# Kernel tuning notes

Hardware: AMD Instinct MI355X
Metric: run time of the kernel (lower is better)

The kernel has to match this reference:

```python
import jax, jax.numpy as jnp
import numpy as np

K_TOP = 2        # experts_per_tok
E_MLP = 8        # num_mlp_experts


def setup_inputs() -> dict:
    key = jax.random.key(0)
    ks = jax.random.split(key, 6)
    B, T, C, H, E_ve, V = 2, 2048, 1024, 2048, 2, 32000
    return {
        "x": jax.random.normal(ks[0], (B, T, C), dtype=jnp.float32),
        "token_ids": jax.random.randint(ks[1], (B, T), 0, V, dtype=jnp.int32),
        "w_up": jax.random.normal(ks[2], (E_MLP, H, C), dtype=jnp.float32) * 0.02,
        "w_down": jax.random.normal(ks[3], (E_MLP, C, H), dtype=jnp.float32) * 0.02,
        "router_w": jax.random.normal(ks[4], (E_MLP + E_ve, C), dtype=jnp.float32) * 0.02,
        "router_bias": jnp.zeros((E_MLP + E_ve,), dtype=jnp.float32),
        "ve_tables": jax.random.normal(ks[5], (E_ve, V, C), dtype=jnp.float32) * 0.02,
    }


def reference(x, token_ids, w_up, w_down, router_w, router_bias, ve_tables):
    B, T, C = x.shape
    N = B * T
    E_total = router_w.shape[0]
    x_flat = x.reshape(N, C)

    # Sigmoid router with aux-loss-free bias (DeepSeekV3 style): select top-k on
    # biased scores, gate with unbiased sigmoid scores normalized over the top-k.
    scores = jax.nn.sigmoid(x_flat @ router_w.T)              # (N, E_total)
    _, top_idx = jax.lax.top_k(scores + router_bias, K_TOP)   # (N, k)
    top_w = jnp.take_along_axis(scores, top_idx, axis=1)      # (N, k)
    top_w = top_w / jnp.sum(top_w, axis=1, keepdims=True)

    rows = jnp.arange(N)[:, None]
    sparse_w = jnp.zeros((N, E_total), dtype=x.dtype).at[rows, top_idx].set(top_w)

    # Dense all-expert FFN (relu^2 activation), then mask by routing weights.
    hidden = jnp.einsum('nc,ehc->enh', x_flat, w_up)          # (E_mlp, N, H)
    hidden = jnp.square(jax.nn.relu(hidden))
    mlp_out = jnp.einsum('enh,ech->enc', hidden, w_down)      # (E_mlp, N, C)
    mlp_contrib = jnp.einsum('enc,ne->nc', mlp_out, sparse_w[:, :E_MLP])

    # VE experts: shared embedding lookups, (E_ve, N, C).
    ve_out = ve_tables[:, token_ids.reshape(N), :]
    ve_contrib = jnp.einsum('enc,ne->nc', ve_out, sparse_w[:, E_MLP:])

    return (mlp_contrib + ve_contrib).reshape(B, T, C)
```

## Files before the change

### kernel.cpp

```cpp
#include <hip/hip_runtime.h>
#include <hip/hip_bf16.h>
#include <stdint.h>

#define N_TOK 4096
#define C_DIM 1024
#define H_DIM 2048
#define V_DIM 32000
#define NE_MLP 8
#define NE_TOT 10

typedef __attribute__((ext_vector_type(8))) short bf16x8;
typedef __attribute__((ext_vector_type(4))) short bf16x4;
typedef __attribute__((ext_vector_type(4))) float f32x4;

#define BM 128
#define BN 128
#define BK 32

__device__ __forceinline__ void gload16(const void* g, void* l) {
    __builtin_amdgcn_global_load_lds(
        (const __attribute__((address_space(1))) void*)g,
        (__attribute__((address_space(3))) void*)l,
        16, 0, 0);
}

__device__ __forceinline__ unsigned short bf16bits(float v) {
    __hip_bfloat16 h = __float2bfloat16(v);
    return *reinterpret_cast<unsigned short*>(&h);
}

__global__ void __launch_bounds__(256) cvt_kernel(
    const float* __restrict__ src, __hip_bfloat16* __restrict__ dst)
{
    const int i = blockIdx.x * 256 + threadIdx.x;
    f32x4 v = reinterpret_cast<const f32x4*>(src)[i];
    bf16x4 b;
    b.x = (short)bf16bits(v.x); b.y = (short)bf16bits(v.y);
    b.z = (short)bf16bits(v.z); b.w = (short)bf16bits(v.w);
    reinterpret_cast<bf16x4*>(dst)[i] = b;
}

__global__ void __launch_bounds__(256) router_kernel(
    const float* __restrict__ x, const float* __restrict__ rw,
    const float* __restrict__ rb, int* __restrict__ tok_list,
    int* __restrict__ te, int* __restrict__ tp, float* __restrict__ tw,
    float* __restrict__ vw, int* __restrict__ cnt)
{
    const int lane = threadIdx.x & 63;
    const int n = blockIdx.x * 4 + (threadIdx.x >> 6);
    const f32x4* xr  = reinterpret_cast<const f32x4*>(x + (size_t)n * C_DIM);
    const f32x4* rw4 = reinterpret_cast<const f32x4*>(rw);

    float acc[NE_TOT];
    #pragma unroll
    for (int e = 0; e < NE_TOT; ++e) acc[e] = 0.f;

    #pragma unroll
    for (int kk = 0; kk < C_DIM / 256; ++kk) {
        f32x4 xv = xr[kk * 64 + lane];
        #pragma unroll
        for (int e = 0; e < NE_TOT; ++e) {
            f32x4 wv = rw4[e * (C_DIM / 4) + kk * 64 + lane];
            acc[e] += xv.x * wv.x + xv.y * wv.y + xv.z * wv.z + xv.w * wv.w;
        }
    }
    #pragma unroll
    for (int e = 0; e < NE_TOT; ++e) {
        for (int m = 32; m > 0; m >>= 1) acc[e] += __shfl_xor(acc[e], m, 64);
    }

    if (lane == 0) {
        float s[NE_TOT], sb[NE_TOT];
        #pragma unroll
        for (int e = 0; e < NE_TOT; ++e) {
            s[e]  = 1.f / (1.f + expf(-acc[e]));
            sb[e] = s[e] + rb[e];
        }
        int i0 = 0;
        #pragma unroll
        for (int e = 1; e < NE_TOT; ++e) if (sb[e] > sb[i0]) i0 = e;
        int i1 = (i0 == 0) ? 1 : 0;
        #pragma unroll
        for (int e = 0; e < NE_TOT; ++e)
            if (e != i0 && sb[e] > sb[i1]) i1 = e;

        float w0 = s[i0], w1 = s[i1];
        float inv = 1.f / (w0 + w1);
        w0 *= inv; w1 *= inv;

        float wv0 = 0.f, wv1 = 0.f;
        int   idx[2] = {i0, i1};
        float wt[2]  = {w0, w1};
        #pragma unroll
        for (int k = 0; k < 2; ++k) {
            if (idx[k] < NE_MLP) {
                int p = atomicAdd(&cnt[idx[k]], 1);
                tok_list[idx[k] * N_TOK + p] = n;
                te[n * 2 + k] = idx[k];
                tp[n * 2 + k] = p;
                tw[n * 2 + k] = wt[k];
            } else {
                te[n * 2 + k] = -1;
                tp[n * 2 + k] = 0;
                tw[n * 2 + k] = 0.f;
                if (idx[k] == NE_MLP) wv0 = wt[k]; else wv1 = wt[k];
            }
        }
        vw[n * 2 + 0] = wv0;
        vw[n * 2 + 1] = wv1;
    }
}

__global__ void scan_kernel(const int* __restrict__ cnt, int* __restrict__ offs)
{
    if (threadIdx.x == 0) {
        int o = 0;
        for (int e = 0; e < NE_MLP; ++e) { offs[e] = o; o += cnt[e]; }
    }
}

__global__ void __launch_bounds__(256) up_kernel(
    const __hip_bfloat16* __restrict__ xb, const __hip_bfloat16* __restrict__ wub,
    const int* __restrict__ tok_list, const int* __restrict__ cnt,
    const int* __restrict__ offs, __hip_bfloat16* __restrict__ hidden)
{
    const int e = blockIdx.z;
    const int count = cnt[e];
    const int m0 = blockIdx.y * BM;
    if (m0 >= count) return;
    const int n0 = blockIdx.x * BN;
    const int base = offs[e];

    __shared__ __hip_bfloat16 lA[BM * BK];
    __shared__ __hip_bfloat16 lB[BN * BK];

    const int tid  = threadIdx.x;
    const int lane = tid & 63;
    const int wv   = tid >> 6;
    const int wm = (wv >> 1) * 64;
    const int wn = (wv & 1) * 64;

    const __hip_bfloat16* ga[2];
    const __hip_bfloat16* gb[2];
    __hip_bfloat16* la[2];
    __hip_bfloat16* lb[2];
    const __hip_bfloat16* wB = wub + (size_t)e * H_DIM * C_DIM;
    #pragma unroll
    for (int t = 0; t < 2; ++t) {
        const int srow = (wv + 4 * t) * 16 + (lane >> 2);
        int r = m0 + srow;
        const int tok = tok_list[e * N_TOK + (r < count ? r : count - 1)];
        ga[t] = xb + (size_t)tok * C_DIM + (lane & 3) * 8;
        gb[t] = wB + (size_t)(n0 + srow) * C_DIM + (lane & 3) * 8;
        la[t] = lA + (wv + 4 * t) * 512;
        lb[t] = lB + (wv + 4 * t) * 512;
    }

    f32x4 acc[4][4];
    #pragma unroll
    for (int i = 0; i < 4; ++i)
        #pragma unroll
        for (int j = 0; j < 4; ++j)
            acc[i][j] = (f32x4){0.f, 0.f, 0.f, 0.f};

    const int fm  = lane & 15;
    const int fkb = (lane >> 4) * 8;

    for (int k0 = 0; k0 < C_DIM; k0 += BK) {
        __syncthreads();
        #pragma unroll
        for (int t = 0; t < 2; ++t) {
            gload16(ga[t], la[t]);
            gload16(gb[t], lb[t]);
            ga[t] += BK; gb[t] += BK;
        }
        __syncthreads();
        bf16x8 af[4], bfr[4];
        #pragma unroll
        for (int i = 0; i < 4; ++i) {
            af[i]  = *reinterpret_cast<const bf16x8*>(lA + (wm + i * 16 + fm) * BK + fkb);
            bfr[i] = *reinterpret_cast<const bf16x8*>(lB + (wn + i * 16 + fm) * BK + fkb);
        }
        #pragma unroll
        for (int i = 0; i < 4; ++i)
            #pragma unroll
            for (int j = 0; j < 4; ++j)
                acc[i][j] = __builtin_amdgcn_mfma_f32_16x16x32_bf16(af[i], bfr[j], acc[i][j], 0, 0, 0);
    }

    const int fr = (lane >> 4) * 4;
    #pragma unroll
    for (int i = 0; i < 4; ++i) {
        #pragma unroll
        for (int r = 0; r < 4; ++r) {
            const int gr = m0 + wm + i * 16 + fr + r;
            const bool ok = gr < count;
            unsigned int pk[4];
            #pragma unroll
            for (int j = 0; j < 4; ++j) {
                float v = acc[i][j][r];
                v = v > 0.f ? v * v : 0.f;
                unsigned short b = bf16bits(v);
                int other = __shfl_xor((int)b, 1, 64);
                pk[j] = (unsigned)b | ((unsigned)other << 16);
            }
            if (ok && !(lane & 1)) {
                __hip_bfloat16* hrow = hidden + (size_t)(base + gr) * H_DIM + n0 + wn + fm;
                #pragma unroll
                for (int j = 0; j < 4; ++j)
                    *reinterpret_cast<unsigned int*>(hrow + j * 16) = pk[j];
            }
        }
    }
}

__global__ void __launch_bounds__(256) down_kernel(
    const __hip_bfloat16* __restrict__ hidden, const __hip_bfloat16* __restrict__ wdb,
    const int* __restrict__ cnt, const int* __restrict__ offs,
    float* __restrict__ mlp_buf)
{
    const int e = blockIdx.z;
    const int count = cnt[e];
    const int m0 = blockIdx.y * BM;
    if (m0 >= count) return;
    const int n0 = blockIdx.x * BN;
    const int base = offs[e];

    __shared__ __hip_bfloat16 lA[BM * BK];
    __shared__ __hip_bfloat16 lB[BN * BK];

    const int tid  = threadIdx.x;
    const int lane = tid & 63;
    const int wv   = tid >> 6;
    const int wm = (wv >> 1) * 64;
    const int wn = (wv & 1) * 64;

    const __hip_bfloat16* ga[2];
    const __hip_bfloat16* gb[2];
    __hip_bfloat16* la[2];
    __hip_bfloat16* lb[2];
    const __hip_bfloat16* wB = wdb + (size_t)e * C_DIM * H_DIM;
    #pragma unroll
    for (int t = 0; t < 2; ++t) {
        const int srow = (wv + 4 * t) * 16 + (lane >> 2);
        int r = m0 + srow;
        const int arow = base + (r < count ? r : count - 1);
        ga[t] = hidden + (size_t)arow * H_DIM + (lane & 3) * 8;
        gb[t] = wB + (size_t)(n0 + srow) * H_DIM + (lane & 3) * 8;
        la[t] = lA + (wv + 4 * t) * 512;
        lb[t] = lB + (wv + 4 * t) * 512;
    }

    f32x4 acc[4][4];
    #pragma unroll
    for (int i = 0; i < 4; ++i)
        #pragma unroll
        for (int j = 0; j < 4; ++j)
            acc[i][j] = (f32x4){0.f, 0.f, 0.f, 0.f};

    const int fm  = lane & 15;
    const int fkb = (lane >> 4) * 8;

    for (int k0 = 0; k0 < H_DIM; k0 += BK) {
        __syncthreads();
        #pragma unroll
        for (int t = 0; t < 2; ++t) {
            gload16(ga[t], la[t]);
            gload16(gb[t], lb[t]);
            ga[t] += BK; gb[t] += BK;
        }
        __syncthreads();
        bf16x8 af[4], bfr[4];
        #pragma unroll
        for (int i = 0; i < 4; ++i) {
            af[i]  = *reinterpret_cast<const bf16x8*>(lA + (wm + i * 16 + fm) * BK + fkb);
            bfr[i] = *reinterpret_cast<const bf16x8*>(lB + (wn + i * 16 + fm) * BK + fkb);
        }
        #pragma unroll
        for (int i = 0; i < 4; ++i)
            #pragma unroll
            for (int j = 0; j < 4; ++j)
                acc[i][j] = __builtin_amdgcn_mfma_f32_16x16x32_bf16(af[i], bfr[j], acc[i][j], 0, 0, 0);
    }

    const int fr = (lane >> 4) * 4;
    #pragma unroll
    for (int i = 0; i < 4; ++i) {
        #pragma unroll
        for (int r = 0; r < 4; ++r) {
            const int gr = m0 + wm + i * 16 + fr + r;
            if (gr < count) {
                float* orow = mlp_buf + (size_t)(base + gr) * C_DIM + n0 + wn + fm;
                #pragma unroll
                for (int j = 0; j < 4; ++j)
                    orow[j * 16] = acc[i][j][r];
            }
        }
    }
}

__global__ void __launch_bounds__(256) combine_kernel(
    const int* __restrict__ token_ids, const float* __restrict__ vt,
    const float* __restrict__ vw, const int* __restrict__ te,
    const int* __restrict__ tp, const float* __restrict__ tw,
    const int* __restrict__ offs, const float* __restrict__ mlp_buf,
    float* __restrict__ out)
{
    const int n = blockIdx.x;
    const int c = threadIdx.x;
    const int t = token_ids[n];
    const float w0 = vw[n * 2 + 0];
    const float w1 = vw[n * 2 + 1];
    f32x4 v = {0.f, 0.f, 0.f, 0.f};
    if (w0 != 0.f)
        v += w0 * reinterpret_cast<const f32x4*>(vt + (size_t)t * C_DIM)[c];
    if (w1 != 0.f)
        v += w1 * reinterpret_cast<const f32x4*>(vt + ((size_t)V_DIM + t) * C_DIM)[c];
    #pragma unroll
    for (int k = 0; k < 2; ++k) {
        const int e = te[n * 2 + k];
        if (e >= 0) {
            const int slot = offs[e] + tp[n * 2 + k];
            v += tw[n * 2 + k] *
                 reinterpret_cast<const f32x4*>(mlp_buf + (size_t)slot * C_DIM)[c];
        }
    }
    reinterpret_cast<f32x4*>(out + (size_t)n * C_DIM)[c] = v;
}

extern "C" void kernel_launch(void* const* d_in, const int* in_sizes, int n_in,
                              void* d_out, int out_size, void* d_ws, size_t ws_size,
                              hipStream_t stream)
{
    const float* x         = (const float*)d_in[0];
    const int*   token_ids = (const int*)  d_in[1];
    const float* w_up      = (const float*)d_in[2];
    const float* w_down    = (const float*)d_in[3];
    const float* router_w  = (const float*)d_in[4];
    const float* router_b  = (const float*)d_in[5];
    const float* ve_tables = (const float*)d_in[6];
    float* out = (float*)d_out;

    char* ws = (char*)d_ws;
    size_t off = 0;
    __hip_bfloat16* hidden  = (__hip_bfloat16*)(ws + off); off += (size_t)8192 * H_DIM * 2;
    float*          mlp_buf = (float*)         (ws + off); off += (size_t)8192 * C_DIM * 4;
    __hip_bfloat16* xb      = (__hip_bfloat16*)(ws + off); off += (size_t)N_TOK * C_DIM * 2;
    __hip_bfloat16* wub     = (__hip_bfloat16*)(ws + off); off += (size_t)NE_MLP * H_DIM * C_DIM * 2;
    __hip_bfloat16* wdb     = (__hip_bfloat16*)(ws + off); off += (size_t)NE_MLP * C_DIM * H_DIM * 2;
    int*   tok_list = (int*)  (ws + off); off += (size_t)NE_MLP * N_TOK * 4;
    int*   te       = (int*)  (ws + off); off += (size_t)N_TOK * 2 * 4;
    int*   tp       = (int*)  (ws + off); off += (size_t)N_TOK * 2 * 4;
    float* tw       = (float*)(ws + off); off += (size_t)N_TOK * 2 * 4;
    float* vw       = (float*)(ws + off); off += (size_t)N_TOK * 2 * 4;
    int*   cnt      = (int*)  (ws + off); off += 64;
    int*   offs     = (int*)  (ws + off);

    hipMemsetAsync(cnt, 0, NE_MLP * sizeof(int), stream);

    cvt_kernel<<<(N_TOK * C_DIM) / 1024, 256, 0, stream>>>(x, xb);
    cvt_kernel<<<(NE_MLP * H_DIM * C_DIM) / 1024, 256, 0, stream>>>(w_up, wub);
    cvt_kernel<<<(NE_MLP * C_DIM * H_DIM) / 1024, 256, 0, stream>>>(w_down, wdb);

    router_kernel<<<N_TOK / 4, 256, 0, stream>>>(x, router_w, router_b,
                                                 tok_list, te, tp, tw, vw, cnt);
    scan_kernel<<<1, 64, 0, stream>>>(cnt, offs);

    up_kernel<<<dim3(H_DIM / BN, N_TOK / BM, NE_MLP), 256, 0, stream>>>(
        xb, wub, tok_list, cnt, offs, hidden);
    down_kernel<<<dim3(C_DIM / BN, N_TOK / BM, NE_MLP), 256, 0, stream>>>(
        hidden, wdb, cnt, offs, mlp_buf);
    combine_kernel<<<N_TOK, 256, 0, stream>>>(token_ids, ve_tables, vw,
                                              te, tp, tw, offs, mlp_buf, out);
}
```

Baseline: 595.4 us.

## Split-K the down GEMM, double K-tile per sync, merge conversions, drop scan

Merges the three fp32-to-bf16 conversion launches into one kernel and removes the scan kernel by giving each expert a fixed N_TOK-row slab. The up and down GEMMs now load two 32-wide K halves per barrier pair, which halves the number of syncs. The down GEMM is split over K into two halves written to separate fp32 slabs, doubling its grid, and the combine kernel sums the two partials. The cost is extra fp32 partial-buffer traffic and a larger workspace.

```diff
diff --git a/kernel.cpp b/kernel.cpp
--- a/kernel.cpp
+++ b/kernel.cpp
@@ -15,7 +15,8 @@
 
 #define BM 128
 #define BN 128
-#define BK 32
+#define HKE 32
+#define HALF_ELEMS (128 * 32)
 
 __device__ __forceinline__ void gload16(const void* g, void* l) {
     __builtin_amdgcn_global_load_lds(
@@ -29,15 +30,25 @@
     return *reinterpret_cast<unsigned short*>(&h);
 }
 
+#define CVT_N0 (N_TOK * C_DIM / 4)
+#define CVT_N1 (NE_MLP * H_DIM * C_DIM / 4)
 __global__ void __launch_bounds__(256) cvt_kernel(
-    const float* __restrict__ src, __hip_bfloat16* __restrict__ dst)
+    const float* __restrict__ x, const float* __restrict__ wu,
+    const float* __restrict__ wd, __hip_bfloat16* __restrict__ xb,
+    __hip_bfloat16* __restrict__ wub, __hip_bfloat16* __restrict__ wdb)
 {
     const int i = blockIdx.x * 256 + threadIdx.x;
-    f32x4 v = reinterpret_cast<const f32x4*>(src)[i];
+    const float* src;
+    __hip_bfloat16* dst;
+    int j;
+    if (i < CVT_N0)            { src = x;  dst = xb;  j = i; }
+    else if (i < CVT_N0 + CVT_N1) { src = wu; dst = wub; j = i - CVT_N0; }
+    else                       { src = wd; dst = wdb; j = i - CVT_N0 - CVT_N1; }
+    f32x4 v = reinterpret_cast<const f32x4*>(src)[j];
     bf16x4 b;
     b.x = (short)bf16bits(v.x); b.y = (short)bf16bits(v.y);
     b.z = (short)bf16bits(v.z); b.w = (short)bf16bits(v.w);
-    reinterpret_cast<bf16x4*>(dst)[i] = b;
+    reinterpret_cast<bf16x4*>(dst)[j] = b;
 }
 
 __global__ void __launch_bounds__(256) router_kernel(
@@ -111,28 +122,19 @@
     }
 }
 
-__global__ void scan_kernel(const int* __restrict__ cnt, int* __restrict__ offs)
-{
-    if (threadIdx.x == 0) {
-        int o = 0;
-        for (int e = 0; e < NE_MLP; ++e) { offs[e] = o; o += cnt[e]; }
-    }
-}
-
 __global__ void __launch_bounds__(256) up_kernel(
     const __hip_bfloat16* __restrict__ xb, const __hip_bfloat16* __restrict__ wub,
     const int* __restrict__ tok_list, const int* __restrict__ cnt,
-    const int* __restrict__ offs, __hip_bfloat16* __restrict__ hidden)
+    __hip_bfloat16* __restrict__ hidden)
 {
     const int e = blockIdx.z;
     const int count = cnt[e];
     const int m0 = blockIdx.y * BM;
     if (m0 >= count) return;
     const int n0 = blockIdx.x * BN;
-    const int base = offs[e];
-
-    __shared__ __hip_bfloat16 lA[BM * BK];
-    __shared__ __hip_bfloat16 lB[BN * BK];
+
+    __shared__ __hip_bfloat16 lA[2 * HALF_ELEMS];
+    __shared__ __hip_bfloat16 lB[2 * HALF_ELEMS];
 
     const int tid  = threadIdx.x;
     const int lane = tid & 63;
@@ -166,26 +168,33 @@
     const int fm  = lane & 15;
     const int fkb = (lane >> 4) * 8;
 
-    for (int k0 = 0; k0 < C_DIM; k0 += BK) {
+    for (int k0 = 0; k0 < C_DIM; k0 += 2 * HKE) {
         __syncthreads();
         #pragma unroll
-        for (int t = 0; t < 2; ++t) {
-            gload16(ga[t], la[t]);
-            gload16(gb[t], lb[t]);
-            ga[t] += BK; gb[t] += BK;
-        }
+        for (int h = 0; h < 2; ++h) {
+            #pragma unroll
+            for (int t = 0; t < 2; ++t) {
+                gload16(ga[t] + h * HKE, la[t] + h * HALF_ELEMS);
+                gload16(gb[t] + h * HKE, lb[t] + h * HALF_ELEMS);
+            }
+        }
+        #pragma unroll
+        for (int t = 0; t < 2; ++t) { ga[t] += 2 * HKE; gb[t] += 2 * HKE; }
         __syncthreads();
-        bf16x8 af[4], bfr[4];
-        #pragma unroll
-        for (int i = 0; i < 4; ++i) {
-            af[i]  = *reinterpret_cast<const bf16x8*>(lA + (wm + i * 16 + fm) * BK + fkb);
-            bfr[i] = *reinterpret_cast<const bf16x8*>(lB + (wn + i * 16 + fm) * BK + fkb);
-        }
-        #pragma unroll
-        for (int i = 0; i < 4; ++i)
-            #pragma unroll
-            for (int j = 0; j < 4; ++j)
-                acc[i][j] = __builtin_amdgcn_mfma_f32_16x16x32_bf16(af[i], bfr[j], acc[i][j], 0, 0, 0);
+        #pragma unroll
+        for (int h = 0; h < 2; ++h) {
+            bf16x8 af[4], bfr[4];
+            #pragma unroll
+            for (int i = 0; i < 4; ++i) {
+                af[i]  = *reinterpret_cast<const bf16x8*>(lA + h * HALF_ELEMS + (wm + i * 16 + fm) * HKE + fkb);
+                bfr[i] = *reinterpret_cast<const bf16x8*>(lB + h * HALF_ELEMS + (wn + i * 16 + fm) * HKE + fkb);
+            }
+            #pragma unroll
+            for (int i = 0; i < 4; ++i)
+                #pragma unroll
+                for (int j = 0; j < 4; ++j)
+                    acc[i][j] = __builtin_amdgcn_mfma_f32_16x16x32_bf16(af[i], bfr[j], acc[i][j], 0, 0, 0);
+        }
     }
 
     const int fr = (lane >> 4) * 4;
@@ -205,7 +214,7 @@
                 pk[j] = (unsigned)b | ((unsigned)other << 16);
             }
             if (ok && !(lane & 1)) {
-                __hip_bfloat16* hrow = hidden + (size_t)(base + gr) * H_DIM + n0 + wn + fm;
+                __hip_bfloat16* hrow = hidden + (size_t)(e * N_TOK + gr) * H_DIM + n0 + wn + fm;
                 #pragma unroll
                 for (int j = 0; j < 4; ++j)
                     *reinterpret_cast<unsigned int*>(hrow + j * 16) = pk[j];
@@ -214,20 +223,21 @@
     }
 }
 
+#define MLP_SLAB ((size_t)NE_MLP * N_TOK * C_DIM)
 __global__ void __launch_bounds__(256) down_kernel(
     const __hip_bfloat16* __restrict__ hidden, const __hip_bfloat16* __restrict__ wdb,
-    const int* __restrict__ cnt, const int* __restrict__ offs,
-    float* __restrict__ mlp_buf)
-{
-    const int e = blockIdx.z;
+    const int* __restrict__ cnt, float* __restrict__ mlp_buf)
+{
+    const int e  = blockIdx.z >> 1;
+    const int kh = blockIdx.z & 1;
     const int count = cnt[e];
     const int m0 = blockIdx.y * BM;
     if (m0 >= count) return;
     const int n0 = blockIdx.x * BN;
-    const int base = offs[e];
-
-    __shared__ __hip_bfloat16 lA[BM * BK];
-    __shared__ __hip_bfloat16 lB[BN * BK];
+    const int kbase = kh * (H_DIM / 2);
+
+    __shared__ __hip_bfloat16 lA[2 * HALF_ELEMS];
+    __shared__ __hip_bfloat16 lB[2 * HALF_ELEMS];
 
     const int tid  = threadIdx.x;
     const int lane = tid & 63;
@@ -244,9 +254,9 @@
     for (int t = 0; t < 2; ++t) {
         const int srow = (wv + 4 * t) * 16 + (lane >> 2);
         int r = m0 + srow;
-        const int arow = base + (r < count ? r : count - 1);
-        ga[t] = hidden + (size_t)arow * H_DIM + (lane & 3) * 8;
-        gb[t] = wB + (size_t)(n0 + srow) * H_DIM + (lane & 3) * 8;
+        const int arow = e * N_TOK + (r < count ? r : count - 1);
+        ga[t] = hidden + (size_t)arow * H_DIM + kbase + (lane & 3) * 8;
+        gb[t] = wB + (size_t)(n0 + srow) * H_DIM + kbase + (lane & 3) * 8;
         la[t] = lA + (wv + 4 * t) * 512;
         lb[t] = lB + (wv + 4 * t) * 512;
     }
@@ -261,28 +271,36 @@
     const int fm  = lane & 15;
     const int fkb = (lane >> 4) * 8;
 
-    for (int k0 = 0; k0 < H_DIM; k0 += BK) {
+    for (int k0 = 0; k0 < H_DIM / 2; k0 += 2 * HKE) {
         __syncthreads();
         #pragma unroll
-        for (int t = 0; t < 2; ++t) {
-            gload16(ga[t], la[t]);
-            gload16(gb[t], lb[t]);
-            ga[t] += BK; gb[t] += BK;
-        }
+        for (int h = 0; h < 2; ++h) {
+            #pragma unroll
+            for (int t = 0; t < 2; ++t) {
+                gload16(ga[t] + h * HKE, la[t] + h * HALF_ELEMS);
+                gload16(gb[t] + h * HKE, lb[t] + h * HALF_ELEMS);
+            }
+        }
+        #pragma unroll
+        for (int t = 0; t < 2; ++t) { ga[t] += 2 * HKE; gb[t] += 2 * HKE; }
         __syncthreads();
-        bf16x8 af[4], bfr[4];
-        #pragma unroll
-        for (int i = 0; i < 4; ++i) {
-            af[i]  = *reinterpret_cast<const bf16x8*>(lA + (wm + i * 16 + fm) * BK + fkb);
-            bfr[i] = *reinterpret_cast<const bf16x8*>(lB + (wn + i * 16 + fm) * BK + fkb);
-        }
-        #pragma unroll
-        for (int i = 0; i < 4; ++i)
-            #pragma unroll
-            for (int j = 0; j < 4; ++j)
-                acc[i][j] = __builtin_amdgcn_mfma_f32_16x16x32_bf16(af[i], bfr[j], acc[i][j], 0, 0, 0);
-    }
-
+        #pragma unroll
+        for (int h = 0; h < 2; ++h) {
+            bf16x8 af[4], bfr[4];
+            #pragma unroll
+            for (int i = 0; i < 4; ++i) {
+                af[i]  = *reinterpret_cast<const bf16x8*>(lA + h * HALF_ELEMS + (wm + i * 16 + fm) * HKE + fkb);
+                bfr[i] = *reinterpret_cast<const bf16x8*>(lB + h * HALF_ELEMS + (wn + i * 16 + fm) * HKE + fkb);
+            }
+            #pragma unroll
+            for (int i = 0; i < 4; ++i)
+                #pragma unroll
+                for (int j = 0; j < 4; ++j)
+                    acc[i][j] = __builtin_amdgcn_mfma_f32_16x16x32_bf16(af[i], bfr[j], acc[i][j], 0, 0, 0);
+        }
+    }
+
+    float* obuf = mlp_buf + (size_t)kh * MLP_SLAB;
     const int fr = (lane >> 4) * 4;
     #pragma unroll
     for (int i = 0; i < 4; ++i) {
@@ -290,7 +308,7 @@
         for (int r = 0; r < 4; ++r) {
             const int gr = m0 + wm + i * 16 + fr + r;
             if (gr < count) {
-                float* orow = mlp_buf + (size_t)(base + gr) * C_DIM + n0 + wn + fm;
+                float* orow = obuf + (size_t)(e * N_TOK + gr) * C_DIM + n0 + wn + fm;
                 #pragma unroll
                 for (int j = 0; j < 4; ++j)
                     orow[j * 16] = acc[i][j][r];
@@ -303,8 +321,7 @@
     const int* __restrict__ token_ids, const float* __restrict__ vt,
     const float* __restrict__ vw, const int* __restrict__ te,
     const int* __restrict__ tp, const float* __restrict__ tw,
-    const int* __restrict__ offs, const float* __restrict__ mlp_buf,
-    float* __restrict__ out)
+    const float* __restrict__ mlp_buf, float* __restrict__ out)
 {
     const int n = blockIdx.x;
     const int c = threadIdx.x;
@@ -320,9 +337,10 @@
     for (int k = 0; k < 2; ++k) {
         const int e = te[n * 2 + k];
         if (e >= 0) {
-            const int slot = offs[e] + tp[n * 2 + k];
-            v += tw[n * 2 + k] *
-                 reinterpret_cast<const f32x4*>(mlp_buf + (size_t)slot * C_DIM)[c];
+            const size_t slot = (size_t)(e * N_TOK + tp[n * 2 + k]) * C_DIM;
+            f32x4 a = reinterpret_cast<const f32x4*>(mlp_buf + slot)[c];
+            f32x4 b = reinterpret_cast<const f32x4*>(mlp_buf + MLP_SLAB + slot)[c];
+            v += tw[n * 2 + k] * (a + b);
         }
     }
     reinterpret_cast<f32x4*>(out + (size_t)n * C_DIM)[c] = v;
@@ -343,8 +361,8 @@
 
     char* ws = (char*)d_ws;
     size_t off = 0;
-    __hip_bfloat16* hidden  = (__hip_bfloat16*)(ws + off); off += (size_t)8192 * H_DIM * 2;
-    float*          mlp_buf = (float*)         (ws + off); off += (size_t)8192 * C_DIM * 4;
+    __hip_bfloat16* hidden  = (__hip_bfloat16*)(ws + off); off += (size_t)NE_MLP * N_TOK * H_DIM * 2;
+    float*          mlp_buf = (float*)         (ws + off); off += 2 * MLP_SLAB * 4;
     __hip_bfloat16* xb      = (__hip_bfloat16*)(ws + off); off += (size_t)N_TOK * C_DIM * 2;
     __hip_bfloat16* wub     = (__hip_bfloat16*)(ws + off); off += (size_t)NE_MLP * H_DIM * C_DIM * 2;
     __hip_bfloat16* wdb     = (__hip_bfloat16*)(ws + off); off += (size_t)NE_MLP * C_DIM * H_DIM * 2;
@@ -354,22 +372,17 @@
     float* tw       = (float*)(ws + off); off += (size_t)N_TOK * 2 * 4;
     float* vw       = (float*)(ws + off); off += (size_t)N_TOK * 2 * 4;
     int*   cnt      = (int*)  (ws + off); off += 64;
-    int*   offs     = (int*)  (ws + off);
 
     hipMemsetAsync(cnt, 0, NE_MLP * sizeof(int), stream);
 
-    cvt_kernel<<<(N_TOK * C_DIM) / 1024, 256, 0, stream>>>(x, xb);
-    cvt_kernel<<<(NE_MLP * H_DIM * C_DIM) / 1024, 256, 0, stream>>>(w_up, wub);
-    cvt_kernel<<<(NE_MLP * C_DIM * H_DIM) / 1024, 256, 0, stream>>>(w_down, wdb);
-
+    cvt_kernel<<<(CVT_N0 + 2 * CVT_N1) / 256, 256, 0, stream>>>(
+        x, w_up, w_down, xb, wub, wdb);
     router_kernel<<<N_TOK / 4, 256, 0, stream>>>(x, router_w, router_b,
                                                  tok_list, te, tp, tw, vw, cnt);
-    scan_kernel<<<1, 64, 0, stream>>>(cnt, offs);
-
     up_kernel<<<dim3(H_DIM / BN, N_TOK / BM, NE_MLP), 256, 0, stream>>>(
-        xb, wub, tok_list, cnt, offs, hidden);
-    down_kernel<<<dim3(C_DIM / BN, N_TOK / BM, NE_MLP), 256, 0, stream>>>(
-        hidden, wdb, cnt, offs, mlp_buf);
+        xb, wub, tok_list, cnt, hidden);
+    down_kernel<<<dim3(C_DIM / BN, N_TOK / BM, NE_MLP * 2), 256, 0, stream>>>(
+        hidden, wdb, cnt, mlp_buf);
     combine_kernel<<<N_TOK, 256, 0, stream>>>(token_ids, ve_tables, vw,
-                                              te, tp, tw, offs, mlp_buf, out);
-}
+                                              te, tp, tw, mlp_buf, out);
+}
```

New measurement: 589.0 us. No clear change (-1.1%).
